# Kernel optimization log

Hardware: AMD Instinct MI355X
Metric: run time of the kernel (lower is better)

## Reference

```python
import jax, jax.numpy as jnp
import numpy as np

CROP_SIZE = 28
NUM_BOXES = 100


def setup_inputs() -> dict:
    key = jax.random.key(0)
    k1, k2 = jax.random.split(key)
    images = jax.random.normal(k1, (8, 512, 512, 32), dtype=jnp.float32)
    boxes = jax.random.uniform(k2, (8, NUM_BOXES, 4), dtype=jnp.float32)
    return {"images": images, "boxes": boxes}


def _crop_and_resize(images, boxes, box_ind, crop_h, crop_w):
    """Faithful port of tf.image.crop_and_resize (bilinear, extrapolation_value=0).

    images: [B,H,W,C], boxes: [N,4] normalized (y1,x1,y2,x2), box_ind: [N] int32.
    Returns [N, crop_h, crop_w, C].
    """
    B, H, W, C = images.shape
    dt = images.dtype
    y1, x1, y2, x2 = boxes[:, 0], boxes[:, 1], boxes[:, 2], boxes[:, 3]
    # TF formula for crop_size > 1
    h_scale = (y2 - y1) * (H - 1) / (crop_h - 1)  # [N]
    w_scale = (x2 - x1) * (W - 1) / (crop_w - 1)
    gy = jnp.arange(crop_h, dtype=dt)
    gx = jnp.arange(crop_w, dtype=dt)
    in_y = y1[:, None] * (H - 1) + gy[None, :] * h_scale[:, None]  # [N,crop_h]
    in_x = x1[:, None] * (W - 1) + gx[None, :] * w_scale[:, None]  # [N,crop_w]
    valid_y = (in_y >= 0) & (in_y <= H - 1)
    valid_x = (in_x >= 0) & (in_x <= W - 1)

    y0f = jnp.floor(in_y)
    x0f = jnp.floor(in_x)
    ly = in_y - y0f  # lerp weights
    lx = in_x - x0f
    y0 = jnp.clip(y0f.astype(jnp.int32), 0, H - 1)
    y1i = jnp.clip(y0 + 1, 0, H - 1)
    x0 = jnp.clip(x0f.astype(jnp.int32), 0, W - 1)
    x1i = jnp.clip(x0 + 1, 0, W - 1)

    b = box_ind[:, None, None]  # [N,1,1]
    # 4 corner gathers, each [N,crop_h,crop_w,C]
    tl = images[b, y0[:, :, None], x0[:, None, :]]
    tr = images[b, y0[:, :, None], x1i[:, None, :]]
    bl = images[b, y1i[:, :, None], x0[:, None, :]]
    br = images[b, y1i[:, :, None], x1i[:, None, :]]

    lxw = lx[:, None, :, None]  # [N,1,crop_w,1]
    lyw = ly[:, :, None, None]  # [N,crop_h,1,1]
    top = tl + (tr - tl) * lxw
    bot = bl + (br - bl) * lxw
    out = top + (bot - top) * lyw

    mask = (valid_y[:, :, None] & valid_x[:, None, :])[..., None]
    return jnp.where(mask, out, jnp.zeros((), dt))


def reference(images, boxes):
    B = images.shape[0]
    box_ind = jnp.repeat(jnp.arange(B, dtype=jnp.int32), NUM_BOXES)  # [B*NUM_BOXES]
    boxes_flat = boxes.reshape(-1, 4)
    return _crop_and_resize(images, boxes_flat, box_ind, CROP_SIZE, CROP_SIZE)
```

## Files before the change

kernel.cpp:

```cpp
#include <hip/hip_runtime.h>

#define CROP   28
#define NBOX   100
#define IMG_H  512
#define IMG_W  512
#define IMG_C  32
#define BATCH  8

typedef float floatx4 __attribute__((ext_vector_type(4)));

__global__ __launch_bounds__(256) void crop_resize_kernel(
    const float* __restrict__ images,
    const float* __restrict__ boxes,
    float* __restrict__ out)
{
    const int tid = blockIdx.x * blockDim.x + threadIdx.x;
    const int total = BATCH * NBOX * CROP * CROP * 4;
    if (tid >= total) return;

    const int q  = tid & 3;
    const int p  = tid >> 2;
    const int x  = p % CROP;
    const int t  = p / CROP;
    const int y  = t % CROP;
    const int n  = t / CROP;
    const int b  = n / NBOX;

    const float by1 = boxes[n * 4 + 0];
    const float bx1 = boxes[n * 4 + 1];
    const float by2 = boxes[n * 4 + 2];
    const float bx2 = boxes[n * 4 + 3];

    const float Hm1 = (float)(IMG_H - 1);
    const float Wm1 = (float)(IMG_W - 1);
    const float h_scale = (by2 - by1) * Hm1 / (float)(CROP - 1);
    const float w_scale = (bx2 - bx1) * Wm1 / (float)(CROP - 1);

    const float in_y = by1 * Hm1 + (float)y * h_scale;
    const float in_x = bx1 * Wm1 + (float)x * w_scale;

    const bool valid = (in_y >= 0.0f) && (in_y <= Hm1) &&
                       (in_x >= 0.0f) && (in_x <= Wm1);

    const float y0f = floorf(in_y);
    const float x0f = floorf(in_x);
    const float ly = in_y - y0f;
    const float lx = in_x - x0f;

    int y0 = (int)y0f; y0 = y0 < 0 ? 0 : (y0 > IMG_H - 1 ? IMG_H - 1 : y0);
    int x0 = (int)x0f; x0 = x0 < 0 ? 0 : (x0 > IMG_W - 1 ? IMG_W - 1 : x0);
    const int y1i = (y0 + 1 < IMG_H - 1) ? y0 + 1 : IMG_H - 1;
    const int x1i = (x0 + 1 < IMG_W - 1) ? x0 + 1 : IMG_W - 1;

    const int C4 = IMG_C / 4;
    const floatx4* img4 = (const floatx4*)images;

    const int rowStride = IMG_W * C4;
    const int imgStride = IMG_H * rowStride;
    const int base = b * imgStride;
    const int r0 = base + y0  * rowStride;
    const int r1 = base + y1i * rowStride;

    const int atl = r0 + x0  * C4 + q;
    const int atr = r0 + x1i * C4 + q;
    const int abl = r1 + x0  * C4 + q;
    const int abr = r1 + x1i * C4 + q;

    const floatx4 tl0 = img4[atl];
    const floatx4 tl1 = img4[atl + 4];
    const floatx4 tr0 = img4[atr];
    const floatx4 tr1 = img4[atr + 4];
    const floatx4 bl0 = img4[abl];
    const floatx4 bl1 = img4[abl + 4];
    const floatx4 br0 = img4[abr];
    const floatx4 br1 = img4[abr + 4];

    const floatx4 top0 = tl0 + (tr0 - tl0) * lx;
    const floatx4 bot0 = bl0 + (br0 - bl0) * lx;
    floatx4 res0 = top0 + (bot0 - top0) * ly;

    const floatx4 top1 = tl1 + (tr1 - tl1) * lx;
    const floatx4 bot1 = bl1 + (br1 - bl1) * lx;
    floatx4 res1 = top1 + (bot1 - top1) * ly;

    if (!valid) {
        res0 = (floatx4)0.0f;
        res1 = (floatx4)0.0f;
    }

    floatx4* dst = ((floatx4*)out) + p * C4 + q;
    __builtin_nontemporal_store(res0, dst);
    __builtin_nontemporal_store(res1, dst + 4);
}

extern "C" void kernel_launch(void* const* d_in, const int* in_sizes, int n_in,
                              void* d_out, int out_size, void* d_ws, size_t ws_size,
                              hipStream_t stream) {
    const float* images = (const float*)d_in[0];
    const float* boxes  = (const float*)d_in[1];
    float* out = (float*)d_out;

    const int total = BATCH * NBOX * CROP * CROP * 4;
    const int block = 256;
    const int grid = (total + block - 1) / block;
    crop_resize_kernel<<<grid, block, 0, stream>>>(images, boxes, out);
}
```

Before: 52.10 us.

## Sort crop row-group tasks by source y to improve cache locality

Adds a per-image bitonic sort kernel that orders 4-row crop tasks by their approximate source image row. The main kernel then walks tasks in that permuted order so neighbouring blocks touch nearby image rows, aiming for better L2/MALL reuse of the gathered corner pixels. This costs an extra kernel launch, a sort run on only 8 blocks, and an indirect perm lookup per thread. It falls back to the unsorted order when the workspace is too small.

```diff
diff --git a/kernel.cpp b/kernel.cpp
--- a/kernel.cpp
+++ b/kernel.cpp
@@ -7,23 +7,81 @@
 #define IMG_C  32
 #define BATCH  8
 
+#define TPB    7
+#define TASKS_PER_IMG (NBOX * TPB)
+#define SORT_N 1024
+#define THREADS_PER_TASK 448
+
 typedef float floatx4 __attribute__((ext_vector_type(4)));
 
+__global__ __launch_bounds__(256) void sort_tasks_kernel(
+    const float* __restrict__ boxes, int* __restrict__ perm)
+{
+    const int img = blockIdx.x;
+    __shared__ float skey[SORT_N];
+    __shared__ int   sval[SORT_N];
+
+    for (int t = threadIdx.x; t < SORT_N; t += 256) {
+        float k = 3.0e38f;
+        int v = 0;
+        if (t < TASKS_PER_IMG) {
+            const int box = t / TPB;
+            const int rg  = t % TPB;
+            const int n   = img * NBOX + box;
+            const float y1 = boxes[n * 4 + 0];
+            const float y2 = boxes[n * 4 + 2];
+            const float hs = (y2 - y1) * (float)(IMG_H - 1) / (float)(CROP - 1);
+            k = y1 * (float)(IMG_H - 1) + ((float)(rg * 4) + 1.5f) * hs;
+            v = n * TPB + rg;
+        }
+        skey[t] = k;
+        sval[t] = v;
+    }
+    __syncthreads();
+
+    for (int k = 2; k <= SORT_N; k <<= 1) {
+        for (int j = k >> 1; j > 0; j >>= 1) {
+            for (int t = threadIdx.x; t < SORT_N; t += 256) {
+                const int ixj = t ^ j;
+                if (ixj > t) {
+                    const bool up = ((t & k) == 0);
+                    const float a = skey[t], b = skey[ixj];
+                    if ((a > b) == up) {
+                        skey[t] = b; skey[ixj] = a;
+                        const int tv = sval[t];
+                        sval[t] = sval[ixj]; sval[ixj] = tv;
+                    }
+                }
+            }
+            __syncthreads();
+        }
+    }
+
+    for (int t = threadIdx.x; t < TASKS_PER_IMG; t += 256)
+        perm[img * TASKS_PER_IMG + t] = sval[t];
+}
+
+template<bool USE_PERM>
 __global__ __launch_bounds__(256) void crop_resize_kernel(
     const float* __restrict__ images,
     const float* __restrict__ boxes,
+    const int*   __restrict__ perm,
     float* __restrict__ out)
 {
     const int tid = blockIdx.x * blockDim.x + threadIdx.x;
-    const int total = BATCH * NBOX * CROP * CROP * 4;
+    const int total = BATCH * TASKS_PER_IMG * THREADS_PER_TASK;
     if (tid >= total) return;
 
-    const int q  = tid & 3;
-    const int p  = tid >> 2;
-    const int x  = p % CROP;
-    const int t  = p / CROP;
-    const int y  = t % CROP;
-    const int n  = t / CROP;
+    const int u = tid / THREADS_PER_TASK;
+    const int r = tid % THREADS_PER_TASK;
+    const int task = USE_PERM ? perm[u] : u;
+    const int n  = task / TPB;
+    const int rg = task % TPB;
+    const int rowin = r / 112;
+    const int rx = r % 112;
+    const int x  = rx >> 2;
+    const int q  = rx & 3;
+    const int y  = rg * 4 + rowin;
     const int b  = n / NBOX;
 
     const float by1 = boxes[n * 4 + 0];
@@ -88,6 +146,7 @@
         res1 = (floatx4)0.0f;
     }
 
+    const int p = n * (CROP * CROP) + y * CROP + x;
     floatx4* dst = ((floatx4*)out) + p * C4 + q;
     __builtin_nontemporal_store(res0, dst);
     __builtin_nontemporal_store(res1, dst + 4);
@@ -99,9 +158,17 @@
     const float* images = (const float*)d_in[0];
     const float* boxes  = (const float*)d_in[1];
     float* out = (float*)d_out;
+    int* perm = (int*)d_ws;
 
-    const int total = BATCH * NBOX * CROP * CROP * 4;
+    const int total = BATCH * TASKS_PER_IMG * THREADS_PER_TASK;
     const int block = 256;
     const int grid = (total + block - 1) / block;
-    crop_resize_kernel<<<grid, block, 0, stream>>>(images, boxes, out);
+
+    const size_t perm_bytes = (size_t)BATCH * TASKS_PER_IMG * sizeof(int);
+    if (ws_size >= perm_bytes) {
+        sort_tasks_kernel<<<BATCH, 256, 0, stream>>>(boxes, perm);
+        crop_resize_kernel<true><<<grid, block, 0, stream>>>(images, boxes, perm, out);
+    } else {
+        crop_resize_kernel<false><<<grid, block, 0, stream>>>(images, boxes, perm, out);
+    }
 }
```

New measurement: 85.15 us. 63.4% more time.
